# Kernel tuning notes

Measured on AMD Instinct MI355X. Metric: run time of the kernel, lower is better.

## Reference

```python
import jax, jax.numpy as jnp
import numpy as np

D_MODEL = 1280
NUM_EXPERTS = 20
HEAD_DIM = D_MODEL // NUM_EXPERTS  # 64
SCALE = HEAD_DIM ** -0.5


def setup_inputs() -> dict:
    key = jax.random.key(0)
    ks = jax.random.split(key, 8)
    B, S = 4, 1024
    s_in = 1.0 / np.sqrt(D_MODEL)
    x = jax.random.normal(ks[0], (B, S, D_MODEL), dtype=jnp.float32)
    # per-expert QKV projections stacked: [E, d_model, 3*head_dim]
    wqkv = jax.random.uniform(ks[1], (NUM_EXPERTS, D_MODEL, 3 * HEAD_DIM), jnp.float32, -s_in, s_in)
    bqkv = jax.random.uniform(ks[2], (NUM_EXPERTS, 3 * HEAD_DIM), jnp.float32, -s_in, s_in)
    router_w = jax.random.uniform(ks[3], (D_MODEL, NUM_EXPERTS), jnp.float32, -s_in, s_in)
    router_b = jax.random.uniform(ks[4], (NUM_EXPERTS,), jnp.float32, -s_in, s_in)
    out_w = jax.random.uniform(ks[5], (D_MODEL, D_MODEL), jnp.float32, -s_in, s_in)
    out_b = jax.random.uniform(ks[6], (D_MODEL,), jnp.float32, -s_in, s_in)
    return {"x": x, "wqkv": wqkv, "bqkv": bqkv, "router_w": router_w,
            "router_b": router_b, "out_w": out_w, "out_b": out_b}


def reference(x, wqkv, bqkv, router_w, router_b, out_w, out_b):
    # x: [B, S, D]
    B, S, D = x.shape
    E, H = NUM_EXPERTS, HEAD_DIM
    # router softmax gates (dropout = identity in eval)
    gates = jax.nn.softmax(x @ router_w + router_b, axis=-1)  # [B, S, E]
    # per-expert QKV: [E, B, S, 3H]
    qkv = jnp.einsum('bsd,edh->ebsh', x, wqkv) + bqkv[:, None, None, :]
    q, k, v = jnp.split(qkv, 3, axis=-1)  # each [E, B, S, H]
    scores = jnp.einsum('ebqh,ebkh->ebqk', q, k) * SCALE  # [E, B, S, S]
    attn = jax.nn.softmax(scores, axis=-1)
    eo = jnp.einsum('ebqk,ebkh->ebqh', attn, v)  # [E, B, S, H]
    # gate multiply and scatter into disjoint feature slices == concat over experts
    eo = eo * jnp.transpose(gates, (2, 0, 1))[..., None]  # [E, B, S, H]
    combined = jnp.transpose(eo, (1, 2, 0, 3)).reshape(B, S, E * H)  # [B, S, D]
    return combined @ out_w + out_b
```

## Files before the change

### kernel.cpp

```cpp
#include <hip/hip_runtime.h>
#include <hip/hip_bf16.h>

#define D_MODEL 1280
#define NUM_EXPERTS 20
#define HEAD_DIM 64
#define SEQ 1024
#define BATCH 4
#define BS_TOK 4096
#define QKV_N 192
#define QKV_W 3840

typedef __attribute__((ext_vector_type(8))) short short8;
typedef __attribute__((ext_vector_type(4))) float f32x4;
typedef __attribute__((ext_vector_type(16))) float f32x16;
typedef __hip_bfloat16 bf16;

static __device__ __forceinline__ void gload_lds16(const void* g, void* l) {
  __builtin_amdgcn_global_load_lds((const __attribute__((address_space(1))) void*)g,
                                   (__attribute__((address_space(3))) void*)l, 16, 0, 0);
}

__global__ __launch_bounds__(256) void k_rwT(const float* __restrict__ in,
                                             float* __restrict__ out) {
  int i = blockIdx.x * 256 + threadIdx.x;
  if (i < D_MODEL * NUM_EXPERTS) {
    int d = i / NUM_EXPERTS, e = i % NUM_EXPERTS;
    out[e * D_MODEL + d] = in[i];
  }
}

__global__ __launch_bounds__(256) void k_gates(const float* __restrict__ x,
    const float* __restrict__ rwT, const float* __restrict__ rb,
    float* __restrict__ gates, bf16* __restrict__ xb)
{
  __shared__ float xs[4][D_MODEL];
  __shared__ float logits[4][NUM_EXPERTS];
  const int r0 = blockIdx.x * 4;
  for (int i = threadIdx.x; i < 4 * (D_MODEL / 2); i += 256) {
    int r = i / (D_MODEL / 2), d2 = (i % (D_MODEL / 2)) * 2;
    float2 v = *(const float2*)(x + (size_t)(r0 + r) * D_MODEL + d2);
    xs[r][d2] = v.x; xs[r][d2 + 1] = v.y;
    __hip_bfloat162 h;
    h.x = __float2bfloat16(v.x); h.y = __float2bfloat16(v.y);
    *(__hip_bfloat162*)(xb + (size_t)(r0 + r) * D_MODEL + d2) = h;
  }
  __syncthreads();
  const int wid = threadIdx.x >> 6, lane = threadIdx.x & 63;
  for (int e = 0; e < NUM_EXPERTS; ++e) {
    float s = 0.f;
    #pragma unroll
    for (int j = 0; j < D_MODEL / 64; ++j) {
      int d = lane + 64 * j;
      s += xs[wid][d] * rwT[e * D_MODEL + d];
    }
    #pragma unroll
    for (int m = 32; m >= 1; m >>= 1) s += __shfl_xor(s, m);
    if (lane == 0) logits[wid][e] = s + rb[e];
  }
  __syncthreads();
  if (lane < 32) {
    float v = (lane < NUM_EXPERTS) ? logits[wid][lane] : -1e30f;
    float mx = v;
    #pragma unroll
    for (int m = 16; m >= 1; m >>= 1) mx = fmaxf(mx, __shfl_xor(mx, m, 32));
    float p = (lane < NUM_EXPERTS) ? __expf(v - mx) : 0.f;
    float sum = p;
    #pragma unroll
    for (int m = 16; m >= 1; m >>= 1) sum += __shfl_xor(sum, m, 32);
    if (lane < NUM_EXPERTS)
      gates[(size_t)(r0 + wid) * NUM_EXPERTS + lane] = p / sum;
  }
}

__global__ __launch_bounds__(256) void k_transpose(const float* __restrict__ in,
    bf16* __restrict__ out, int R, int C)
{
  __shared__ float tile[32][33];
  const size_t bo = (size_t)blockIdx.z * R * C;
  const int c0 = blockIdx.x * 32, r0 = blockIdx.y * 32;
  const int tx = threadIdx.x, ty = threadIdx.y;
  #pragma unroll
  for (int i = 0; i < 4; ++i)
    tile[ty + 8*i][tx] = in[bo + (size_t)(r0 + ty + 8*i) * C + (c0 + tx)];
  __syncthreads();
  #pragma unroll
  for (int i = 0; i < 4; ++i)
    out[bo + (size_t)(c0 + ty + 8*i) * R + (r0 + tx)] =
        __float2bfloat16(tile[tx][ty + 8*i]);
}

__global__ __launch_bounds__(512, 2) void k_gemm256(
    const bf16* __restrict__ A, const bf16* __restrict__ BT,
    const float* __restrict__ bias, bf16* __restrict__ C,
    int M, int N, int K)
{
  __shared__ __align__(16) bf16 lds[4][2][256 * 32];
  const int bid = blockIdx.x;
  const int xcd = bid & 7, c = bid >> 3;
  const int m0 = (xcd * 2 + (c & 1)) * 256;
  const int n0 = (c >> 1) * 256;
  const int tid = threadIdx.x, wid = tid >> 6, lane = tid & 63;
  const int wr = wid >> 2, wcn = wid & 3;
  const int fr = lane & 15, fg = lane >> 4;
  const int nt = K / 32;

  auto STAGE = [&](int t, int buf) {
    const bf16* Ag = A + (size_t)m0 * K + t * 32;
    const bf16* Bg = BT + (size_t)n0 * K + t * 32;
    #pragma unroll
    for (int i = 0; i < 2; ++i) {
      int idx = i * 512 + tid;
      int row = idx >> 2, sc = idx & 3;
      int g = sc ^ ((row >> 1) & 3);
      gload_lds16(Ag + (size_t)row * K + g * 8, &lds[buf][0][idx * 8]);
    }
    #pragma unroll
    for (int i = 0; i < 2; ++i) {
      int idx = i * 512 + tid;
      int row = idx >> 2, sc = idx & 3;
      int g = sc ^ ((row >> 1) & 3);
      gload_lds16(Bg + (size_t)row * K + g * 8, &lds[buf][1][idx * 8]);
    }
  };

  f32x4 acc[8][4] = {};
  auto COMPUTE = [&](int buf) {
    const bf16* As_ = &lds[buf][0][0];
    const bf16* Bs_ = &lds[buf][1][0];
    short8 af[8], bfv[4];
    #pragma unroll
    for (int mi = 0; mi < 8; ++mi) {
      int row = wr * 128 + mi * 16 + fr;
      int slot = fg ^ ((row >> 1) & 3);
      af[mi] = *(const short8*)(As_ + row * 32 + slot * 8);
    }
    #pragma unroll
    for (int ni = 0; ni < 4; ++ni) {
      int row = wcn * 64 + ni * 16 + fr;
      int slot = fg ^ ((row >> 1) & 3);
      bfv[ni] = *(const short8*)(Bs_ + row * 32 + slot * 8);
    }
    __builtin_amdgcn_s_setprio(1);
    #pragma unroll
    for (int mi = 0; mi < 8; ++mi) {
      #pragma unroll
      for (int ni = 0; ni < 4; ++ni)
        acc[mi][ni] = __builtin_amdgcn_mfma_f32_16x16x32_bf16(
            af[mi], bfv[ni], acc[mi][ni], 0, 0, 0);
    }
    __builtin_amdgcn_s_setprio(0);
  };

  STAGE(0, 0); STAGE(1, 1); STAGE(2, 2);
  asm volatile("s_waitcnt vmcnt(8)" ::: "memory");
  __builtin_amdgcn_s_barrier();
  __builtin_amdgcn_sched_barrier(0);
  int buf = 0;
  for (int t = 0; t < nt - 3; ++t) {
    int nb = buf + 3; nb = (nb >= 4) ? nb - 4 : nb;
    STAGE(t + 3, nb);
    COMPUTE(buf);
    asm volatile("s_waitcnt vmcnt(8)" ::: "memory");
    __builtin_amdgcn_s_barrier();
    __builtin_amdgcn_sched_barrier(0);
    buf = (buf == 3) ? 0 : buf + 1;
  }
  COMPUTE(buf);
  asm volatile("s_waitcnt vmcnt(4)" ::: "memory");
  __builtin_amdgcn_s_barrier();
  __builtin_amdgcn_sched_barrier(0);
  buf = (buf == 3) ? 0 : buf + 1;
  COMPUTE(buf);
  asm volatile("s_waitcnt vmcnt(0)" ::: "memory");
  __builtin_amdgcn_s_barrier();
  __builtin_amdgcn_sched_barrier(0);
  buf = (buf == 3) ? 0 : buf + 1;
  COMPUTE(buf);

  #pragma unroll
  for (int mi = 0; mi < 8; ++mi) {
    const int gr = m0 + wr * 128 + mi * 16 + fg * 4;
    #pragma unroll
    for (int ni = 0; ni < 4; ++ni) {
      const int gc = n0 + wcn * 64 + ni * 16 + fr;
      const float bv = bias[gc];
      #pragma unroll
      for (int r = 0; r < 4; ++r)
        C[(size_t)(gr + r) * N + gc] = __float2bfloat16(acc[mi][ni][r] + bv);
    }
  }
}

__global__ __launch_bounds__(512, 2) void k_gemm128r(
    const bf16* __restrict__ A, const bf16* __restrict__ BT,
    const float* __restrict__ bias, float* __restrict__ C,
    int M, int N, int K)
{
  __shared__ __align__(16) bf16 lds[4][2][128 * 32];
  const int bid = blockIdx.x;
  const int xcd = bid & 7, c = bid >> 3;
  const int m0 = (xcd * 4 + (c & 3)) * 128;
  const int n0 = (c >> 2) * 128;
  const int tid = threadIdx.x, wid = tid >> 6, lane = tid & 63;
  const int wr = wid >> 2, wcn = wid & 3;
  const int fr = lane & 15, fg = lane >> 4;
  const int nt = K / 32;

  auto STAGE = [&](int t, int buf) {
    const bf16* Ag = A + (size_t)m0 * K + t * 32;
    const bf16* Bg = BT + (size_t)n0 * K + t * 32;
    int row = tid >> 2, sc = tid & 3;
    int g = sc ^ ((row >> 1) & 3);
    gload_lds16(Ag + (size_t)row * K + g * 8, &lds[buf][0][tid * 8]);
    gload_lds16(Bg + (size_t)row * K + g * 8, &lds[buf][1][tid * 8]);
  };

  f32x4 acc[4][2] = {};
  auto COMPUTE = [&](int buf) {
    const bf16* As_ = &lds[buf][0][0];
    const bf16* Bs_ = &lds[buf][1][0];
    short8 af[4], bfv[2];
    #pragma unroll
    for (int mi = 0; mi < 4; ++mi) {
      int row = wr * 64 + mi * 16 + fr;
      int slot = fg ^ ((row >> 1) & 3);
      af[mi] = *(const short8*)(As_ + row * 32 + slot * 8);
    }
    #pragma unroll
    for (int ni = 0; ni < 2; ++ni) {
      int row = wcn * 32 + ni * 16 + fr;
      int slot = fg ^ ((row >> 1) & 3);
      bfv[ni] = *(const short8*)(Bs_ + row * 32 + slot * 8);
    }
    __builtin_amdgcn_s_setprio(1);
    #pragma unroll
    for (int mi = 0; mi < 4; ++mi) {
      #pragma unroll
      for (int ni = 0; ni < 2; ++ni)
        acc[mi][ni] = __builtin_amdgcn_mfma_f32_16x16x32_bf16(
            af[mi], bfv[ni], acc[mi][ni], 0, 0, 0);
    }
    __builtin_amdgcn_s_setprio(0);
  };

  STAGE(0, 0); STAGE(1, 1); STAGE(2, 2);
  asm volatile("s_waitcnt vmcnt(4)" ::: "memory");
  __builtin_amdgcn_s_barrier();
  __builtin_amdgcn_sched_barrier(0);
  int buf = 0;
  for (int t = 0; t < nt - 3; ++t) {
    int nb = buf + 3; nb = (nb >= 4) ? nb - 4 : nb;
    STAGE(t + 3, nb);
    COMPUTE(buf);
    asm volatile("s_waitcnt vmcnt(4)" ::: "memory");
    __builtin_amdgcn_s_barrier();
    __builtin_amdgcn_sched_barrier(0);
    buf = (buf == 3) ? 0 : buf + 1;
  }
  COMPUTE(buf);
  asm volatile("s_waitcnt vmcnt(2)" ::: "memory");
  __builtin_amdgcn_s_barrier();
  __builtin_amdgcn_sched_barrier(0);
  buf = (buf == 3) ? 0 : buf + 1;
  COMPUTE(buf);
  asm volatile("s_waitcnt vmcnt(0)" ::: "memory");
  __builtin_amdgcn_s_barrier();
  __builtin_amdgcn_sched_barrier(0);
  buf = (buf == 3) ? 0 : buf + 1;
  COMPUTE(buf);

  #pragma unroll
  for (int mi = 0; mi < 4; ++mi) {
    const int gr = m0 + wr * 64 + mi * 16 + fg * 4;
    #pragma unroll
    for (int ni = 0; ni < 2; ++ni) {
      const int gc = n0 + wcn * 32 + ni * 16 + fr;
      const float bv = bias[gc];
      #pragma unroll
      for (int r = 0; r < 4; ++r)
        C[(size_t)(gr + r) * N + gc] = acc[mi][ni][r] + bv;
    }
  }
}

__global__ __launch_bounds__(256, 4) void k_attn(
    const bf16* __restrict__ qkv, const float* __restrict__ gates,
    bf16* __restrict__ combined)
{
  __shared__ __align__(16) bf16 Ks[2][64 * 64];
  __shared__ __align__(16) bf16 VTs[64 * 64];
  __shared__ float Ltab[64];
  const int id = blockIdx.x;
  const int xcd = id & 7, kgrp = id >> 3;
  const int qt = kgrp / 10, bel = kgrp - qt * 10;
  const int be = xcd * 10 + bel;
  const int e = be >> 2, b = be & 3;
  const int s0 = qt * 64;
  const int tid = threadIdx.x, wid = tid >> 6, lane = tid & 63;
  const int l31 = lane & 31, hi = lane >> 5;
  const int qw = wid & 1, kh = wid >> 1;
  const bf16* base = qkv + (size_t)(b * SEQ) * QKV_W + e * QKV_N;
  const int rq = s0 + qw * 32 + l31;
  short8 qf[4];
  #pragma unroll
  for (int kc = 0; kc < 4; ++kc)
    qf[kc] = *(const short8*)(base + (size_t)rq * QKV_W + kc*16 + hi*8);
  f32x16 o0 = {}, o1 = {};
  float Lr = 0.f;
  const float CSC = 0.125f * 1.44269504f;

  const int kst_row = (lane >> 3);
  short8 vreg[2];
  auto KSTAGE = [&](int c0, int bsel) {
    #pragma unroll
    for (int p = 0; p < 2; ++p) {
      int W = p*4 + wid;
      int row = W*8 + kst_row;
      int g = (lane & 7) ^ W ^ kst_row;
      gload_lds16(base + (size_t)(c0 + row)*QKV_W + 64 + g*8,
                  &Ks[bsel][(W*64 + lane)*8]);
    }
  };
  auto VLOAD = [&](int c0) {
    #pragma unroll
    for (int it = 0; it < 2; ++it) {
      int key = it*32 + (tid >> 3);
      vreg[it] = *(const short8*)(base + (size_t)(c0 + key)*QKV_W + 128 + (tid & 7)*8);
    }
  };
  auto VWRITE = [&]() {
    #pragma unroll
    for (int it = 0; it < 2; ++it) {
      int key = it*32 + (tid >> 3);
      int h0b = tid & 7;
      int kc_ = key >> 3, ko = key & 7;
      union { short8 v; bf16 hh[8]; } u; u.v = vreg[it];
      #pragma unroll
      for (int j = 0; j < 8; ++j) {
        int scn = kc_ ^ h0b ^ j;
        VTs[(h0b*8 + j)*64 + scn*8 + ko] = u.hh[j];
      }
    }
  };

  KSTAGE(0, 0); VLOAD(0);
  int bsel = 0;
  const int krow = kh*32 + l31;
  const int Sk = ((krow >> 3) ^ krow) & 7;
  for (int t = 0; t < SEQ / 64; ++t) {
    if (t) __syncthreads();
    VWRITE();
    __syncthreads();
    if (t < SEQ / 64 - 1) { KSTAGE((t + 1) * 64, bsel ^ 1); VLOAD((t + 1) * 64); }
    f32x16 sc = {};
    __builtin_amdgcn_s_setprio(1);
    #pragma unroll
    for (int kc = 0; kc < 4; ++kc) {
      int st = (kc*2 + hi) ^ Sk;
      short8 kf = *(const short8*)(&Ks[bsel][krow*64 + st*8]);
      sc = __builtin_amdgcn_mfma_f32_32x32x16_bf16(kf, qf[kc], sc, 0, 0, 0);
    }
    __builtin_amdgcn_s_setprio(0);
    float p[16]; float ls = 0.f;
    #pragma unroll
    for (int i = 0; i < 16; ++i) { p[i] = exp2f(sc[i]*CSC); ls += p[i]; }
    Lr += ls + __shfl_xor(ls, 32);
    union { int w[4]; short8 v; } pf0, pf1;
    int ta, tb;
    asm("v_cvt_pk_bf16_f32 %0, %1, %2" : "=v"(ta) : "v"(p[0]), "v"(p[1]));
    asm("v_cvt_pk_bf16_f32 %0, %1, %2" : "=v"(tb) : "v"(p[4]), "v"(p[5]));
    asm volatile("v_permlane32_swap_b32 %0, %1" : "+v"(ta), "+v"(tb));
    pf0.w[0] = ta; pf0.w[2] = tb;
    asm("v_cvt_pk_bf16_f32 %0, %1, %2" : "=v"(ta) : "v"(p[2]), "v"(p[3]));
    asm("v_cvt_pk_bf16_f32 %0, %1, %2" : "=v"(tb) : "v"(p[6]), "v"(p[7]));
    asm volatile("v_permlane32_swap_b32 %0, %1" : "+v"(ta), "+v"(tb));
    pf0.w[1] = ta; pf0.w[3] = tb;
    asm("v_cvt_pk_bf16_f32 %0, %1, %2" : "=v"(ta) : "v"(p[8]), "v"(p[9]));
    asm("v_cvt_pk_bf16_f32 %0, %1, %2" : "=v"(tb) : "v"(p[12]), "v"(p[13]));
    asm volatile("v_permlane32_swap_b32 %0, %1" : "+v"(ta), "+v"(tb));
    pf1.w[0] = ta; pf1.w[2] = tb;
    asm("v_cvt_pk_bf16_f32 %0, %1, %2" : "=v"(ta) : "v"(p[10]), "v"(p[11]));
    asm("v_cvt_pk_bf16_f32 %0, %1, %2" : "=v"(tb) : "v"(p[14]), "v"(p[15]));
    asm volatile("v_permlane32_swap_b32 %0, %1" : "+v"(ta), "+v"(tb));
    pf1.w[1] = ta; pf1.w[3] = tb;
    __builtin_amdgcn_s_setprio(1);
    #pragma unroll
    for (int kb = 0; kb < 2; ++kb) {
      const short8 pv = (kb == 0) ? pf0.v : pf1.v;
      #pragma unroll
      for (int hb = 0; hb < 2; ++hb) {
        int h = hb*32 + l31;
        int cc = (kh*4 + kb*2 + hi) ^ (((h >> 3) ^ h) & 7);
        short8 vf = *(const short8*)(&VTs[h*64 + cc*8]);
        if (hb == 0) o0 = __builtin_amdgcn_mfma_f32_32x32x16_bf16(pv, vf, o0, 0, 0, 0);
        else         o1 = __builtin_amdgcn_mfma_f32_32x32x16_bf16(pv, vf, o1, 0, 0, 0);
      }
    }
    __builtin_amdgcn_s_setprio(0);
    bsel ^= 1;
  }
  __syncthreads();
  float* Ops = (float*)&Ks[0][0];
  float* Lp  = (float*)&VTs[0];
  if (kh == 1) {
    #pragma unroll
    for (int reg = 0; reg < 16; ++reg) {
      int crow = (reg & 3) + 8*(reg >> 2) + 4*hi;
      Ops[(qw*32 + crow)*64 + l31]      = o0[reg];
      Ops[(qw*32 + crow)*64 + 32 + l31] = o1[reg];
    }
    if (lane < 32) Lp[qw*32 + lane] = Lr;
  }
  __syncthreads();
  if (kh == 0) {
    #pragma unroll
    for (int reg = 0; reg < 16; ++reg) {
      int crow = (reg & 3) + 8*(reg >> 2) + 4*hi;
      o0[reg] += Ops[(qw*32 + crow)*64 + l31];
      o1[reg] += Ops[(qw*32 + crow)*64 + 32 + l31];
    }
    if (lane < 32) {
      float Lt = Lr + Lp[qw*32 + lane];
      float g = gates[(size_t)(b*SEQ + s0 + qw*32 + lane) * NUM_EXPERTS + e];
      Ltab[qw*32 + lane] = g / Lt;
    }
    const int rowbase = b*SEQ + s0 + qw*32;
    #pragma unroll
    for (int reg = 0; reg < 16; ++reg) {
      int crow = (reg & 3) + 8*(reg >> 2) + 4*hi;
      float inv = Ltab[qw*32 + crow];
      combined[(size_t)(rowbase + crow)*D_MODEL + e*64 + l31] =
          __float2bfloat16(o0[reg] * inv);
      combined[(size_t)(rowbase + crow)*D_MODEL + e*64 + 32 + l31] =
          __float2bfloat16(o1[reg] * inv);
    }
  }
}

extern "C" void kernel_launch(void* const* d_in, const int* in_sizes, int n_in,
                              void* d_out, int out_size, void* d_ws, size_t ws_size,
                              hipStream_t stream) {
  const float* x    = (const float*)d_in[0];
  const float* wqkv = (const float*)d_in[1];
  const float* bqkv = (const float*)d_in[2];
  const float* rw   = (const float*)d_in[3];
  const float* rb   = (const float*)d_in[4];
  const float* ow   = (const float*)d_in[5];
  const float* ob   = (const float*)d_in[6];
  char* ws = (char*)d_ws;
  bf16*  xb    = (bf16*)(ws);
  bf16*  wqkvT = (bf16*)(ws + 10485760);
  bf16*  owT   = (bf16*)(ws + 20316160);
  float* gates = (float*)(ws + 23592960);
  bf16*  qkv   = (bf16*)(ws + 23920640);
  bf16*  comb  = (bf16*)(ws + 55377920);
  float* rwT   = (float*)comb;

  k_rwT<<<(D_MODEL * NUM_EXPERTS + 255) / 256, 256, 0, stream>>>(rw, rwT);
  k_gates<<<1024, 256, 0, stream>>>(x, rwT, rb, gates, xb);
  k_transpose<<<dim3(6, 40, 20), dim3(32, 8), 0, stream>>>(wqkv, wqkvT, D_MODEL, QKV_N);
  k_transpose<<<dim3(40, 40, 1), dim3(32, 8), 0, stream>>>(ow, owT, D_MODEL, D_MODEL);
  k_gemm256<<<240, 512, 0, stream>>>(xb, wqkvT, bqkv, qkv, BS_TOK, QKV_W, D_MODEL);
  k_attn<<<1280, 256, 0, stream>>>(qkv, gates, comb);
  k_gemm128r<<<320, 512, 0, stream>>>(comb, owT, ob, (float*)d_out,
                                      BS_TOK, D_MODEL, D_MODEL);
}
```

Baseline: 154.1 us.

## Interleave GEMM staging with MFMA pieces, merge transposes, vectorize router dot

Both GEMM kernels now split each k-step's compute into sub-phases. Each sub-phase issues one piece of the next tile's global-to-LDS loads and runs a small group of MFMAs, with barriers in between. The goal is to spread memory issue across the compute instead of bursting it up front. The two weight-transpose launches are merged into one launch; most blocks in the wqkv portion of the grid return immediately. The router dot product in k_gates now uses float4 loads. The extra per-piece barriers and lgkmcnt waits add synchronization that could stall the MFMA pipeline.

```diff
diff --git a/kernel.cpp b/kernel.cpp
--- a/kernel.cpp
+++ b/kernel.cpp
@@ -33,7 +33,7 @@
     const float* __restrict__ rwT, const float* __restrict__ rb,
     float* __restrict__ gates, bf16* __restrict__ xb)
 {
-  __shared__ float xs[4][D_MODEL];
+  __shared__ __align__(16) float xs[4][D_MODEL];
   __shared__ float logits[4][NUM_EXPERTS];
   const int r0 = blockIdx.x * 4;
   for (int i = threadIdx.x; i < 4 * (D_MODEL / 2); i += 256) {
@@ -49,9 +49,11 @@
   for (int e = 0; e < NUM_EXPERTS; ++e) {
     float s = 0.f;
     #pragma unroll
-    for (int j = 0; j < D_MODEL / 64; ++j) {
-      int d = lane + 64 * j;
-      s += xs[wid][d] * rwT[e * D_MODEL + d];
+    for (int j = 0; j < D_MODEL / 256; ++j) {
+      int d = (lane + 64 * j) * 4;
+      float4 xv = *(const float4*)&xs[wid][d];
+      float4 wv = *(const float4*)&rwT[e * D_MODEL + d];
+      s += xv.x * wv.x + xv.y * wv.y + xv.z * wv.z + xv.w * wv.w;
     }
     #pragma unroll
     for (int m = 32; m >= 1; m >>= 1) s += __shfl_xor(s, m);
@@ -72,20 +74,29 @@
   }
 }
 
-__global__ __launch_bounds__(256) void k_transpose(const float* __restrict__ in,
-    bf16* __restrict__ out, int R, int C)
+__global__ __launch_bounds__(256) void k_transpose2(
+    const float* __restrict__ wqkv, bf16* __restrict__ wqkvT,
+    const float* __restrict__ ow, bf16* __restrict__ owT)
 {
+  const int z = blockIdx.z;
+  const float* in; bf16* out; int R, C;
+  if (z < NUM_EXPERTS) {
+    if (blockIdx.x >= 6) return;
+    in = wqkv + (size_t)z * D_MODEL * QKV_N; out = wqkvT + (size_t)z * D_MODEL * QKV_N;
+    R = D_MODEL; C = QKV_N;
+  } else {
+    in = ow; out = owT; R = D_MODEL; C = D_MODEL;
+  }
   __shared__ float tile[32][33];
-  const size_t bo = (size_t)blockIdx.z * R * C;
   const int c0 = blockIdx.x * 32, r0 = blockIdx.y * 32;
   const int tx = threadIdx.x, ty = threadIdx.y;
   #pragma unroll
   for (int i = 0; i < 4; ++i)
-    tile[ty + 8*i][tx] = in[bo + (size_t)(r0 + ty + 8*i) * C + (c0 + tx)];
+    tile[ty + 8*i][tx] = in[(size_t)(r0 + ty + 8*i) * C + (c0 + tx)];
   __syncthreads();
   #pragma unroll
   for (int i = 0; i < 4; ++i)
-    out[bo + (size_t)(c0 + ty + 8*i) * R + (r0 + tx)] =
+    out[(size_t)(c0 + ty + 8*i) * R + (r0 + tx)] =
         __float2bfloat16(tile[tx][ty + 8*i]);
 }
 
@@ -104,78 +115,86 @@
   const int fr = lane & 15, fg = lane >> 4;
   const int nt = K / 32;
 
-  auto STAGE = [&](int t, int buf) {
-    const bf16* Ag = A + (size_t)m0 * K + t * 32;
-    const bf16* Bg = BT + (size_t)n0 * K + t * 32;
-    #pragma unroll
-    for (int i = 0; i < 2; ++i) {
-      int idx = i * 512 + tid;
-      int row = idx >> 2, sc = idx & 3;
-      int g = sc ^ ((row >> 1) & 3);
-      gload_lds16(Ag + (size_t)row * K + g * 8, &lds[buf][0][idx * 8]);
-    }
-    #pragma unroll
-    for (int i = 0; i < 2; ++i) {
-      int idx = i * 512 + tid;
-      int row = idx >> 2, sc = idx & 3;
-      int g = sc ^ ((row >> 1) & 3);
-      gload_lds16(Bg + (size_t)row * K + g * 8, &lds[buf][1][idx * 8]);
-    }
+  auto STAGE_PIECE = [&](int t, int buf, int p) {
+    const int mat = p >> 1, half = p & 1;
+    const bf16* G = (mat == 0 ? A + (size_t)m0 * K : BT + (size_t)n0 * K)
+                    + (size_t)t * 32;
+    int idx = half * 512 + tid;
+    int row = idx >> 2, sc = idx & 3;
+    int g = sc ^ ((row >> 1) & 3);
+    gload_lds16(G + (size_t)row * K + g * 8, &lds[buf][mat][idx * 8]);
   };
 
   f32x4 acc[8][4] = {};
-  auto COMPUTE = [&](int buf) {
+  auto COMPUTE4 = [&](int buf, int stage_t, int nb, bool do_stage) {
     const bf16* As_ = &lds[buf][0][0];
     const bf16* Bs_ = &lds[buf][1][0];
-    short8 af[8], bfv[4];
-    #pragma unroll
-    for (int mi = 0; mi < 8; ++mi) {
-      int row = wr * 128 + mi * 16 + fr;
-      int slot = fg ^ ((row >> 1) & 3);
-      af[mi] = *(const short8*)(As_ + row * 32 + slot * 8);
-    }
-    #pragma unroll
-    for (int ni = 0; ni < 4; ++ni) {
-      int row = wcn * 64 + ni * 16 + fr;
-      int slot = fg ^ ((row >> 1) & 3);
-      bfv[ni] = *(const short8*)(Bs_ + row * 32 + slot * 8);
-    }
-    __builtin_amdgcn_s_setprio(1);
-    #pragma unroll
-    for (int mi = 0; mi < 8; ++mi) {
+    short8 bfv[4];
+    #pragma unroll
+    for (int p = 0; p < 4; ++p) {
+      short8 af0, af1;
+      {
+        int row = wr * 128 + (2*p) * 16 + fr;
+        af0 = *(const short8*)(As_ + row * 32 + (fg ^ ((row >> 1) & 3)) * 8);
+      }
+      {
+        int row = wr * 128 + (2*p + 1) * 16 + fr;
+        af1 = *(const short8*)(As_ + row * 32 + (fg ^ ((row >> 1) & 3)) * 8);
+      }
+      if (p == 0) {
+        #pragma unroll
+        for (int ni = 0; ni < 4; ++ni) {
+          int row = wcn * 64 + ni * 16 + fr;
+          bfv[ni] = *(const short8*)(Bs_ + row * 32 + (fg ^ ((row >> 1) & 3)) * 8);
+        }
+      }
+      if (do_stage) STAGE_PIECE(stage_t, nb, p);
+      __builtin_amdgcn_s_barrier();
+      asm volatile("s_waitcnt lgkmcnt(0)" ::: "memory");
+      __builtin_amdgcn_sched_barrier(0);
+      __builtin_amdgcn_s_setprio(1);
       #pragma unroll
       for (int ni = 0; ni < 4; ++ni)
-        acc[mi][ni] = __builtin_amdgcn_mfma_f32_16x16x32_bf16(
-            af[mi], bfv[ni], acc[mi][ni], 0, 0, 0);
-    }
-    __builtin_amdgcn_s_setprio(0);
-  };
-
-  STAGE(0, 0); STAGE(1, 1); STAGE(2, 2);
+        acc[2*p][ni] = __builtin_amdgcn_mfma_f32_16x16x32_bf16(
+            af0, bfv[ni], acc[2*p][ni], 0, 0, 0);
+      #pragma unroll
+      for (int ni = 0; ni < 4; ++ni)
+        acc[2*p+1][ni] = __builtin_amdgcn_mfma_f32_16x16x32_bf16(
+            af1, bfv[ni], acc[2*p+1][ni], 0, 0, 0);
+      __builtin_amdgcn_s_setprio(0);
+      __builtin_amdgcn_s_barrier();
+    }
+  };
+
+  #pragma unroll
+  for (int p = 0; p < 4; ++p) STAGE_PIECE(0, 0, p);
+  #pragma unroll
+  for (int p = 0; p < 4; ++p) STAGE_PIECE(1, 1, p);
+  #pragma unroll
+  for (int p = 0; p < 4; ++p) STAGE_PIECE(2, 2, p);
   asm volatile("s_waitcnt vmcnt(8)" ::: "memory");
   __builtin_amdgcn_s_barrier();
   __builtin_amdgcn_sched_barrier(0);
   int buf = 0;
   for (int t = 0; t < nt - 3; ++t) {
     int nb = buf + 3; nb = (nb >= 4) ? nb - 4 : nb;
-    STAGE(t + 3, nb);
-    COMPUTE(buf);
+    COMPUTE4(buf, t + 3, nb, true);
     asm volatile("s_waitcnt vmcnt(8)" ::: "memory");
     __builtin_amdgcn_s_barrier();
     __builtin_amdgcn_sched_barrier(0);
     buf = (buf == 3) ? 0 : buf + 1;
   }
-  COMPUTE(buf);
+  COMPUTE4(buf, 0, 0, false);
   asm volatile("s_waitcnt vmcnt(4)" ::: "memory");
   __builtin_amdgcn_s_barrier();
   __builtin_amdgcn_sched_barrier(0);
   buf = (buf == 3) ? 0 : buf + 1;
-  COMPUTE(buf);
+  COMPUTE4(buf, 0, 0, false);
   asm volatile("s_waitcnt vmcnt(0)" ::: "memory");
   __builtin_amdgcn_s_barrier();
   __builtin_amdgcn_sched_barrier(0);
   buf = (buf == 3) ? 0 : buf + 1;
-  COMPUTE(buf);
+  COMPUTE4(buf, 0, 0, false);
 
   #pragma unroll
   for (int mi = 0; mi < 8; ++mi) {
@@ -206,68 +225,84 @@
   const int fr = lane & 15, fg = lane >> 4;
   const int nt = K / 32;
 
-  auto STAGE = [&](int t, int buf) {
-    const bf16* Ag = A + (size_t)m0 * K + t * 32;
-    const bf16* Bg = BT + (size_t)n0 * K + t * 32;
+  auto STAGE_PIECE = [&](int t, int buf, int p) {
+    const bf16* G = (p == 0 ? A + (size_t)m0 * K : BT + (size_t)n0 * K)
+                    + (size_t)t * 32;
     int row = tid >> 2, sc = tid & 3;
     int g = sc ^ ((row >> 1) & 3);
-    gload_lds16(Ag + (size_t)row * K + g * 8, &lds[buf][0][tid * 8]);
-    gload_lds16(Bg + (size_t)row * K + g * 8, &lds[buf][1][tid * 8]);
+    gload_lds16(G + (size_t)row * K + g * 8, &lds[buf][p][tid * 8]);
   };
 
   f32x4 acc[4][2] = {};
-  auto COMPUTE = [&](int buf) {
+  auto COMPUTE2 = [&](int buf, int stage_t, int nb, bool do_stage) {
     const bf16* As_ = &lds[buf][0][0];
     const bf16* Bs_ = &lds[buf][1][0];
-    short8 af[4], bfv[2];
-    #pragma unroll
-    for (int mi = 0; mi < 4; ++mi) {
-      int row = wr * 64 + mi * 16 + fr;
-      int slot = fg ^ ((row >> 1) & 3);
-      af[mi] = *(const short8*)(As_ + row * 32 + slot * 8);
-    }
-    #pragma unroll
-    for (int ni = 0; ni < 2; ++ni) {
-      int row = wcn * 32 + ni * 16 + fr;
-      int slot = fg ^ ((row >> 1) & 3);
-      bfv[ni] = *(const short8*)(Bs_ + row * 32 + slot * 8);
-    }
-    __builtin_amdgcn_s_setprio(1);
-    #pragma unroll
-    for (int mi = 0; mi < 4; ++mi) {
+    short8 bfv[2];
+    #pragma unroll
+    for (int p = 0; p < 2; ++p) {
+      short8 af0, af1;
+      {
+        int row = wr * 64 + (2*p) * 16 + fr;
+        af0 = *(const short8*)(As_ + row * 32 + (fg ^ ((row >> 1) & 3)) * 8);
+      }
+      {
+        int row = wr * 64 + (2*p + 1) * 16 + fr;
+        af1 = *(const short8*)(As_ + row * 32 + (fg ^ ((row >> 1) & 3)) * 8);
+      }
+      if (p == 0) {
+        #pragma unroll
+        for (int ni = 0; ni < 2; ++ni) {
+          int row = wcn * 32 + ni * 16 + fr;
+          bfv[ni] = *(const short8*)(Bs_ + row * 32 + (fg ^ ((row >> 1) & 3)) * 8);
+        }
+      }
+      if (do_stage) STAGE_PIECE(stage_t, nb, p);
+      __builtin_amdgcn_s_barrier();
+      asm volatile("s_waitcnt lgkmcnt(0)" ::: "memory");
+      __builtin_amdgcn_sched_barrier(0);
+      __builtin_amdgcn_s_setprio(1);
       #pragma unroll
       for (int ni = 0; ni < 2; ++ni)
-        acc[mi][ni] = __builtin_amdgcn_mfma_f32_16x16x32_bf16(
-            af[mi], bfv[ni], acc[mi][ni], 0, 0, 0);
-    }
-    __builtin_amdgcn_s_setprio(0);
-  };
-
-  STAGE(0, 0); STAGE(1, 1); STAGE(2, 2);
+        acc[2*p][ni] = __builtin_amdgcn_mfma_f32_16x16x32_bf16(
+            af0, bfv[ni], acc[2*p][ni], 0, 0, 0);
+      #pragma unroll
+      for (int ni = 0; ni < 2; ++ni)
+        acc[2*p+1][ni] = __builtin_amdgcn_mfma_f32_16x16x32_bf16(
+            af1, bfv[ni], acc[2*p+1][ni], 0, 0, 0);
+      __builtin_amdgcn_s_setprio(0);
+      __builtin_amdgcn_s_barrier();
+    }
+  };
+
+  #pragma unroll
+  for (int p = 0; p < 2; ++p) STAGE_PIECE(0, 0, p);
+  #pragma unroll
+  for (int p = 0; p < 2; ++p) STAGE_PIECE(1, 1, p);
+  #pragma unroll
+  for (int p = 0; p < 2; ++p) STAGE_PIECE(2, 2, p);
   asm volatile("s_waitcnt vmcnt(4)" ::: "memory");
   __builtin_amdgcn_s_barrier();
   __builtin_amdgcn_sched_barrier(0);
   int buf = 0;
   for (int t = 0; t < nt - 3; ++t) {
     int nb = buf + 3; nb = (nb >= 4) ? nb - 4 : nb;
-    STAGE(t + 3, nb);
-    COMPUTE(buf);
+    COMPUTE2(buf, t + 3, nb, true);
     asm volatile("s_waitcnt vmcnt(4)" ::: "memory");
     __builtin_amdgcn_s_barrier();
     __builtin_amdgcn_sched_barrier(0);
     buf = (buf == 3) ? 0 : buf + 1;
   }
-  COMPUTE(buf);
+  COMPUTE2(buf, 0, 0, false);
   asm volatile("s_waitcnt vmcnt(2)" ::: "memory");
   __builtin_amdgcn_s_barrier();
   __builtin_amdgcn_sched_barrier(0);
   buf = (buf == 3) ? 0 : buf + 1;
-  COMPUTE(buf);
+  COMPUTE2(buf, 0, 0, false);
   asm volatile("s_waitcnt vmcnt(0)" ::: "memory");
   __builtin_amdgcn_s_barrier();
   __builtin_amdgcn_sched_barrier(0);
   buf = (buf == 3) ? 0 : buf + 1;
-  COMPUTE(buf);
+  COMPUTE2(buf, 0, 0, false);
 
   #pragma unroll
   for (int mi = 0; mi < 4; ++mi) {
@@ -458,8 +493,7 @@
 
   k_rwT<<<(D_MODEL * NUM_EXPERTS + 255) / 256, 256, 0, stream>>>(rw, rwT);
   k_gates<<<1024, 256, 0, stream>>>(x, rwT, rb, gates, xb);
-  k_transpose<<<dim3(6, 40, 20), dim3(32, 8), 0, stream>>>(wqkv, wqkvT, D_MODEL, QKV_N);
-  k_transpose<<<dim3(40, 40, 1), dim3(32, 8), 0, stream>>>(ow, owT, D_MODEL, D_MODEL);
+  k_transpose2<<<dim3(40, 40, 21), dim3(32, 8), 0, stream>>>(wqkv, wqkvT, ow, owT);
   k_gemm256<<<240, 512, 0, stream>>>(xb, wqkvT, bqkv, qkv, BS_TOK, QKV_W, D_MODEL);
   k_attn<<<1280, 256, 0, stream>>>(qkv, gates, comb);
   k_gemm128r<<<320, 512, 0, stream>>>(comb, owT, ob, (float*)d_out,
```

Measured after the change: 155.3 us. Within noise of the previous version (+0.8%).

## Vectorize gate dot products, merge weight transposes, pack V-transpose LDS writes

Applied to the files above, without the earlier changes.

The router dot product in the gate kernel now reads float4 vectors from LDS and global memory instead of scalars. The two weight-transpose launches are merged into one launch with a 21-slice grid, where the expert slices exit early for out-of-range x tiles. In the attention kernel, each thread now loads two adjacent V rows and writes packed 32-bit pairs into the transposed V tile, replacing single bf16 LDS stores. Together these cut instruction count, LDS store count and launch overhead, at the cost of many idle blocks in the merged transpose grid.

```diff
diff --git a/kernel.cpp b/kernel.cpp
--- a/kernel.cpp
+++ b/kernel.cpp
@@ -33,7 +33,7 @@
     const float* __restrict__ rwT, const float* __restrict__ rb,
     float* __restrict__ gates, bf16* __restrict__ xb)
 {
-  __shared__ float xs[4][D_MODEL];
+  __shared__ __align__(16) float xs[4][D_MODEL];
   __shared__ float logits[4][NUM_EXPERTS];
   const int r0 = blockIdx.x * 4;
   for (int i = threadIdx.x; i < 4 * (D_MODEL / 2); i += 256) {
@@ -49,9 +49,11 @@
   for (int e = 0; e < NUM_EXPERTS; ++e) {
     float s = 0.f;
     #pragma unroll
-    for (int j = 0; j < D_MODEL / 64; ++j) {
-      int d = lane + 64 * j;
-      s += xs[wid][d] * rwT[e * D_MODEL + d];
+    for (int j = 0; j < D_MODEL / 256; ++j) {
+      int d = (lane + 64 * j) * 4;
+      float4 xv = *(const float4*)&xs[wid][d];
+      float4 wv = *(const float4*)&rwT[e * D_MODEL + d];
+      s += xv.x * wv.x + xv.y * wv.y + xv.z * wv.z + xv.w * wv.w;
     }
     #pragma unroll
     for (int m = 32; m >= 1; m >>= 1) s += __shfl_xor(s, m);
@@ -72,20 +74,29 @@
   }
 }
 
-__global__ __launch_bounds__(256) void k_transpose(const float* __restrict__ in,
-    bf16* __restrict__ out, int R, int C)
+__global__ __launch_bounds__(256) void k_transpose2(
+    const float* __restrict__ wqkv, bf16* __restrict__ wqkvT,
+    const float* __restrict__ ow, bf16* __restrict__ owT)
 {
+  const int z = blockIdx.z;
+  const float* in; bf16* out; int R, C;
+  if (z < NUM_EXPERTS) {
+    if (blockIdx.x >= 6) return;
+    in = wqkv + (size_t)z * D_MODEL * QKV_N; out = wqkvT + (size_t)z * D_MODEL * QKV_N;
+    R = D_MODEL; C = QKV_N;
+  } else {
+    in = ow; out = owT; R = D_MODEL; C = D_MODEL;
+  }
   __shared__ float tile[32][33];
-  const size_t bo = (size_t)blockIdx.z * R * C;
   const int c0 = blockIdx.x * 32, r0 = blockIdx.y * 32;
   const int tx = threadIdx.x, ty = threadIdx.y;
   #pragma unroll
   for (int i = 0; i < 4; ++i)
-    tile[ty + 8*i][tx] = in[bo + (size_t)(r0 + ty + 8*i) * C + (c0 + tx)];
+    tile[ty + 8*i][tx] = in[(size_t)(r0 + ty + 8*i) * C + (c0 + tx)];
   __syncthreads();
   #pragma unroll
   for (int i = 0; i < 4; ++i)
-    out[bo + (size_t)(c0 + ty + 8*i) * R + (r0 + tx)] =
+    out[(size_t)(c0 + ty + 8*i) * R + (r0 + tx)] =
         __float2bfloat16(tile[tx][ty + 8*i]);
 }
 
@@ -310,7 +321,8 @@
   const float CSC = 0.125f * 1.44269504f;
 
   const int kst_row = (lane >> 3);
-  short8 vreg[2];
+  const int vkp = tid >> 3, vq4 = tid & 7;
+  short8 vrega, vregb;
   auto KSTAGE = [&](int c0, int bsel) {
     #pragma unroll
     for (int p = 0; p < 2; ++p) {
@@ -322,24 +334,18 @@
     }
   };
   auto VLOAD = [&](int c0) {
-    #pragma unroll
-    for (int it = 0; it < 2; ++it) {
-      int key = it*32 + (tid >> 3);
-      vreg[it] = *(const short8*)(base + (size_t)(c0 + key)*QKV_W + 128 + (tid & 7)*8);
-    }
+    vrega = *(const short8*)(base + (size_t)(c0 + 2*vkp)*QKV_W + 128 + vq4*8);
+    vregb = *(const short8*)(base + (size_t)(c0 + 2*vkp + 1)*QKV_W + 128 + vq4*8);
   };
   auto VWRITE = [&]() {
-    #pragma unroll
-    for (int it = 0; it < 2; ++it) {
-      int key = it*32 + (tid >> 3);
-      int h0b = tid & 7;
-      int kc_ = key >> 3, ko = key & 7;
-      union { short8 v; bf16 hh[8]; } u; u.v = vreg[it];
-      #pragma unroll
-      for (int j = 0; j < 8; ++j) {
-        int scn = kc_ ^ h0b ^ j;
-        VTs[(h0b*8 + j)*64 + scn*8 + ko] = u.hh[j];
-      }
+    const int kc_ = (2*vkp) >> 3, ko0 = (2*vkp) & 7;
+    #pragma unroll
+    for (int j = 0; j < 8; ++j) {
+      int h = vq4*8 + j;
+      int sc = kc_ ^ (vq4 ^ j);
+      unsigned int pk = ((unsigned short)vrega[j]) |
+                        (((unsigned int)(unsigned short)vregb[j]) << 16);
+      *(unsigned int*)&VTs[h*64 + sc*8 + ko0] = pk;
     }
   };
 
@@ -458,8 +464,7 @@
 
   k_rwT<<<(D_MODEL * NUM_EXPERTS + 255) / 256, 256, 0, stream>>>(rw, rwT);
   k_gates<<<1024, 256, 0, stream>>>(x, rwT, rb, gates, xb);
-  k_transpose<<<dim3(6, 40, 20), dim3(32, 8), 0, stream>>>(wqkv, wqkvT, D_MODEL, QKV_N);
-  k_transpose<<<dim3(40, 40, 1), dim3(32, 8), 0, stream>>>(ow, owT, D_MODEL, D_MODEL);
+  k_transpose2<<<dim3(40, 40, 21), dim3(32, 8), 0, stream>>>(wqkv, wqkvT, ow, owT);
   k_gemm256<<<240, 512, 0, stream>>>(xb, wqkvT, bqkv, qkv, BS_TOK, QKV_W, D_MODEL);
   k_attn<<<1280, 256, 0, stream>>>(qkv, gates, comb);
   k_gemm128r<<<320, 512, 0, stream>>>(comb, owT, ob, (float*)d_out,
```

After: 153.8 us (median of 2 runs). Within noise of the previous version (-0.2%).
